# Kernel tuning notes

Measured on AMD Instinct MI355X. Metric: run time of the kernel, lower is better.

Reference implementation:

```python
import jax, jax.numpy as jnp
from jax import lax
import numpy as np

DT = jnp.float32
M = 1000          # quadrature points (torch.linspace steps=1000)
PI = float(np.pi)
EPS = 1e-12       # guards sqrt args against round-off (original asserts instead)


def _trapz(f, x):
    dx = x[1:] - x[:-1]
    return jnp.sum(0.5 * (f[..., 1:] + f[..., :-1]) * dx, axis=-1)


def _ygrid():
    return jnp.linspace(0.001, 0.999, M, dtype=DT)


def _extend(y, integ):
    # prepend linearly-extrapolated value at y=0, append 0 at y=1 (as in torch code)
    slope = (integ[..., 1] - integ[..., 0]) / (y[1] - y[0])
    v0 = integ[..., 0] - slope * y[0]
    yy = jnp.concatenate([jnp.zeros((1,), DT), y, jnp.ones((1,), DT)])
    zrs = jnp.zeros(integ.shape[:-1] + (1,), DT)
    ii = jnp.concatenate([v0[..., None], integ, zrs], axis=-1)
    return yy, ii


def eval_f(a, z):
    _a = jnp.concatenate([jnp.ones((1,), DT), a])  # [1, a0, a1]
    out = jnp.zeros_like(z)
    for i in range(3):
        for j in range(3):
            c = _a[i] * _a[j]
            if i + j == 4:
                out = out - 4.0 * c * z**4 * jnp.log(z)
            else:
                out = out + 4.0 * c * (z**4 - z**(i + j)) / (i + j - 4)
    return out


def eval_df(a, z):
    _a = jnp.concatenate([jnp.ones((1,), DT), a])
    out = jnp.zeros_like(z)
    for i in range(3):
        for j in range(3):
            out = out - 4.0 * _a[i] * _a[j] * z**(i + j)
    return (out + 4.0 * eval_f(a, z)) / z


def _bcoef(a, b):
    last = a.sum() - b.sum()
    return jnp.concatenate([jnp.ones((1,), DT), b, last[None]])  # length 4


def eval_b_(a, b, z):
    c = _bcoef(a, b)
    out = jnp.zeros_like(z)
    for i in range(4):
        for j in range(4):
            out = out + c[i] * c[j] * z**(i + j)
    return out


def eval_db(a, b, z):
    c = _bcoef(a, b)
    x = jnp.zeros_like(z)
    dx = jnp.zeros_like(z)
    for i in range(4):
        x = x + c[i] * z**i
    for i in range(1, 4):
        dx = dx + i * c[i] * z**(i - 1)
    return 2.0 * dx * x


def eval_g(a, b, z):
    return eval_b_(a, b, z) / ((1 - z) * (1 + z) * (1 + z**2))


def eval_dg(a, b, z):
    D = (1 - z) * (1 + z) * (1 + z**2)  # = 1 - z^4
    return eval_db(a, b, z) / D + 4.0 * z**3 * eval_b_(a, b, z) / D**2


def integrate_L(a, b, zs):
    y = _ygrid()
    zs_ = zs[..., None]
    z = zs_ * (1 - y) * (1 + y)
    sqrtg = jnp.sqrt(eval_g(a, b, z))
    f_over_fs = eval_f(a, z) / eval_f(a, zs_)
    arg = f_over_fs / ((1 - y)**4 * (1 + y)**4) - 1.0
    integ = sqrtg / jnp.sqrt(jnp.maximum(arg, EPS)) * y
    yy, ii = _extend(y, integ)
    return 4.0 * zs * _trapz(ii, yy) / PI


def integrate_dL(a, b, zs):
    y = _ygrid()
    zs_ = zs[..., None]
    z = zs_ * (1 - y) * (1 + y)
    fs = eval_f(a, zs_)
    g = eval_g(a, b, z)
    f_over_fs = eval_f(a, z) / fs
    df = eval_df(a, z)
    dfs = eval_df(a, zs_)
    dg = eval_dg(a, b, z)
    r4 = zs_**4 / z**4
    integ = r4 * f_over_fs * (zs_ * dfs / fs + 2 + z * dg / g) - zs_**4 / z**3 * df / fs - 2 - z * dg / g
    integ = integ * 2 * jnp.sqrt(jnp.maximum(1 - z / zs_, 0.0)) * jnp.sqrt(g) / jnp.maximum(r4 * f_over_fs - 1, EPS)**1.5
    yy, ii = _extend(y, integ)
    return _trapz(ii, yy) / PI


def integrate_V(a, b, logcoef, zs):
    coef = jnp.exp(logcoef)
    # connected piece
    y = _ygrid()
    zs_ = zs[..., None]
    z = zs_ * (1 - y) * (1 + y)
    f = eval_f(a, z)
    fg = f * eval_g(a, b, z)
    f_over_fs = f / eval_f(a, zs_)
    w = (1 - y)**2 * (1 + y)**2
    integ = jnp.sqrt(jnp.maximum(fg, EPS)) / w * (1.0 / jnp.sqrt(jnp.maximum(1 - w**2 / f_over_fs, EPS)) - 1.0) * y
    yy, ii = _extend(y, integ)
    Vc = coef * PI * 4.0 * _trapz(ii, yy) / zs
    # disconnected piece
    y2 = jnp.linspace(0.001, 1.0, M, dtype=DT)
    z2 = 1 - (1 - zs_) * y2
    fg2 = eval_f(a, z2) * eval_g(a, b, z2)
    integ2 = jnp.sqrt(jnp.maximum(fg2, EPS)) / z2**2
    yy2 = jnp.concatenate([jnp.zeros((1,), DT), y2])
    ii2 = jnp.concatenate([jnp.ones(integ2.shape[:-1] + (1,), DT), integ2], axis=-1)
    Vd = coef * PI * 2.0 * (1 - zs) * _trapz(ii2, yy2)
    return Vc - Vd


def _bisect(fun, lo, hi, iters=30):
    # keeps invariant fun(lo) >= 0 > fun(hi); matches the torch bisections
    def body(_, c):
        lo, hi = c
        mid = 0.5 * (lo + hi)
        pred = fun(mid) < 0
        return (jnp.where(pred, lo, mid), jnp.where(pred, mid, hi))
    lo, hi = lax.fori_loop(0, iters, body, (jnp.asarray(lo, DT), jnp.asarray(hi, DT)))
    return 0.5 * (lo + hi)


def get_L_max(a, b):
    zs = _bisect(lambda m: integrate_dL(a, b, m), 0.001, 0.999)
    return zs, integrate_L(a, b, zs)


def get_L_crit(a, b, logcoef, zs_max):
    zs = _bisect(lambda m: -integrate_V(a, b, logcoef, m), 0.001, zs_max)
    return zs, integrate_L(a, b, zs)


def find_zs_newton(a, b, L, init, steps=25):
    @jax.checkpoint
    def step(zs, _):
        Lz = integrate_L(a, b, zs)
        dL = integrate_dL(a, b, zs)
        zs = jnp.clip(zs - (Lz - L) / dL, 1e-4, 0.9995)
        return zs, None
    zs, _ = lax.scan(step, init, None, length=steps)
    return zs


def forward(Ls, a, b, logcoef):
    # bisection searches run under torch.no_grad in the original -> stop gradients
    a_ng = lax.stop_gradient(a)
    b_ng = lax.stop_gradient(b)
    lc_ng = lax.stop_gradient(logcoef)
    zs_max, L_max = get_L_max(a_ng, b_ng)
    zs_crit, L_crit = get_L_crit(a_ng, b_ng, lc_ng, zs_max)
    valid = Ls < L_crit
    L_eff = jnp.where(valid, Ls, 0.5 * L_crit)  # masked rows still solve a well-posed problem
    init = jnp.clip(L_eff / L_max * zs_max, 1e-4, 0.9995)  # interp1d through (0,0)-(L_max, zs_max)
    zs = find_zs_newton(a, b, L_eff, init)
    V = integrate_V(a, b, logcoef, zs)
    return jnp.where(valid, V, jnp.zeros_like(V))


def setup_inputs() -> dict:
    key = jax.random.key(0)
    k1, k2, k3 = jax.random.split(key, 3)
    B = 4096
    Ls = jax.random.uniform(k1, (B,), dtype=jnp.float32) * 0.2
    a = 0.05 * jax.random.normal(k2, (2,), dtype=jnp.float32)
    b = 0.05 * jax.random.normal(k3, (2,), dtype=jnp.float32)
    logcoef = jnp.zeros((), jnp.float32)
    return {"Ls": Ls, "a": a, "b": b, "logcoef": logcoef}


def reference(Ls, a, b, logcoef):
    return forward(Ls, a, b, logcoef)
```

## Files before the change

### kernel.cpp

```cpp
#include <hip/hip_runtime.h>
#include <math.h>

#define MQ 1000
#define PI_F 3.14159265358979323846f
#define EPSF 1e-12f
#define DYF  ((float)(0.998/999.0))
#define DY2F ((float)(0.999/999.0))
#define NG   2048
#define HG   (0.998f / (float)NG)

__device__ __forceinline__ float frcp(float x)  { return __builtin_amdgcn_rcpf(x); }
__device__ __forceinline__ float frsq(float x)  { return __builtin_amdgcn_rsqf(x); }
__device__ __forceinline__ float fsqrt(float x) { return __builtin_amdgcn_sqrtf(x); }


struct Co {
    float q1, q2, q3, q4, cf4;
    float e1, e2, e3, e4;
    float b0, b1, p3;
    float coef;
};

__device__ __forceinline__ Co make_co(const float* a, const float* b, const float* lc) {
    Co c;
    float a0 = a[0], a1 = a[1];
    float cf1 = -8.f * a0 / 3.f;
    float cf2 = -2.f * (2.f * a1 + a0 * a0);
    float cf3 = -8.f * a0 * a1;
    c.cf4 = -4.f * a1 * a1;
    c.q1 = -cf1; c.q2 = -cf2; c.q3 = -cf3; c.q4 = cf1 + cf2 + cf3 - 1.f;
    c.e1 = 2.f * a0;
    c.e2 = 2.f * a1 + a0 * a0;
    c.e3 = 2.f * a0 * a1;
    c.e4 = a1 * a1;
    c.b0 = b[0]; c.b1 = b[1];
    c.p3 = a0 + a1 - b[0] - b[1];
    c.coef = expf(lc[0]);
    return c;
}

struct Uni { float zs, fs, rfs, A4; };

__device__ __forceinline__ Uni make_uni(const Co& c, float zs) {
    Uni U; U.zs = zs;
    float z = zs;
    float lg = __logf(z);
    float t4 = c.q4 + c.cf4 * lg;
    float fz = 1.f + z * (c.q1 + z * (c.q2 + z * (c.q3 + z * t4)));
    float s  = 1.f + z * (c.e1 + z * (c.e2 + z * (c.e3 + z * c.e4)));
    U.fs = fz;
    U.rfs = frcp(fz);
    float dfs = 4.f * (fz - s) * frcp(z);
    U.A4 = zs * dfs * U.rfs - 2.f;
    return U;
}

__device__ __forceinline__ void point_LdL(const Co& c, const Uni& U,
                                          float y, float u,
                                          float& iL, float& iD) {
    float u2  = u * u;
    float ru2 = frcp(u2);
    float ru4 = ru2 * ru2;
    float z  = U.zs * u;
    float z2 = z * z, z4 = z2 * z2;
    float lg = __logf(z);
    float t4 = c.q4 + c.cf4 * lg;
    float fz = 1.f + z * (c.q1 + z * (c.q2 + z * (c.q3 + z * t4)));
    float s  = 1.f + z * (c.e1 + z * (c.e2 + z * (c.e3 + z * c.e4)));
    float P  = 1.f + z * (c.b0 + z * (c.b1 + z * c.p3));
    float dP = c.b0 + z * (2.f * c.b1 + z * (3.f * c.p3));
    float D  = 1.f - z4;
    float rsqD = frsq(D);
    float rcpD = rsqD * rsqD;
    float rcpP = frcp(P);
    float zdgg = 2.f * z * dP * rcpP + 4.f * z4 * rcpD;
    float F4 = fz * U.rfs * ru4;
    float S4 = s  * U.rfs * ru4;
    float den = fmaxf(F4 - 1.f, EPSF);
    float rs  = frsq(den);
    float sqg = P * rsqD;
    float t1  = sqg * rs;
    iL = t1 * y;
    float t = F4 * (U.A4 + zdgg) + 4.f * S4 - 2.f - zdgg;
    float rs2 = rs * rs;
    iD = t * (2.f * y) * (t1 * rs2);
}

__device__ __forceinline__ float point_Vc(const Co& c, const Uni& U,
                                          float y, float u) {
    float u2  = u * u;
    float u4  = u2 * u2;
    float ru2 = frcp(u2);
    float z  = U.zs * u;
    float z2 = z * z, z4 = z2 * z2;
    float lg = __logf(z);
    float t4 = c.q4 + c.cf4 * lg;
    float fz = 1.f + z * (c.q1 + z * (c.q2 + z * (c.q3 + z * t4)));
    float P  = 1.f + z * (c.b0 + z * (c.b1 + z * c.p3));
    float D  = 1.f - z4;
    float rsqD = frsq(D);
    float rcpD = rsqD * rsqD;
    float fg = fz * P * P * rcpD;
    float sqfg = fsqrt(fmaxf(fg, EPSF));
    float rfz = frcp(fz);
    float arg = fmaxf(1.f - u4 * U.fs * rfz, EPSF);
    float t = frsq(arg) - 1.f;
    return sqfg * ru2 * t * y;
}

__device__ __forceinline__ float point_Vd(const Co& c, const Uni& U, float y2) {
    float z  = 1.f - (1.f - U.zs) * y2;
    float z2 = z * z, z4 = z2 * z2;
    float lg = __logf(z);
    float t4 = c.q4 + c.cf4 * lg;
    float fz = 1.f + z * (c.q1 + z * (c.q2 + z * (c.q3 + z * t4)));
    float P  = 1.f + z * (c.b0 + z * (c.b1 + z * c.p3));
    float D  = 1.f - z4;
    float rsqD = frsq(D);
    float fg = fz * P * P * (rsqD * rsqD);
    float sq = fsqrt(fmaxf(fg, EPSF));
    float rz = frcp(z);
    return sq * rz * rz;
}

__device__ __forceinline__ float trapz_ext(float S, float i0, float i1, float iN) {
    float slope = (i1 - i0) * frcp(DYF);
    float v0 = i0 - slope * 0.001f;
    float yLast = 0.001f + 999.f * DYF;
    return DYF * (S - 0.5f * (i0 + iN))
         + 0.5f * (v0 + i0) * 0.001f
         + 0.5f * iN * (1.f - yLast);
}

__device__ __forceinline__ float trapz_d(float S, float q0, float qN) {
    return 0.5f * (1.f + q0) * 0.001f + DY2F * (S - 0.5f * (q0 + qN));
}

__device__ __forceinline__ void wave_LdL(const Co& c, const Uni& U, int lane,
                                         float& Lout, float& dLout) {
    float sL = 0.f, sD = 0.f, l0 = 0.f, d0 = 0.f, lN = 0.f, dN = 0.f;
#pragma unroll
    for (int k = 0; k < 16; ++k) {
        if (k < 15 || lane < 40) {
            int j = lane + 64 * k;
            float y = fmaf((float)j, DYF, 0.001f);
            float u = 1.f - y * y;
            float iL, iD;
            point_LdL(c, U, y, u, iL, iD);
            sL += iL; sD += iD;
            if (k == 0)  { l0 = iL; d0 = iD; }
            if (k == 15) { lN = iL; dN = iD; }
        }
    }
#pragma unroll
    for (int o = 32; o > 0; o >>= 1) {
        sL += __shfl_xor(sL, o, 64);
        sD += __shfl_xor(sD, o, 64);
    }
    float i0 = __shfl(l0, 0, 64), i1 = __shfl(l0, 1, 64), iN = __shfl(lN, 39, 64);
    float e0 = __shfl(d0, 0, 64), e1 = __shfl(d0, 1, 64), eN = __shfl(dN, 39, 64);
    Lout  = 4.f * U.zs * trapz_ext(sL, i0, i1, iN) / PI_F;
    dLout = trapz_ext(sD, e0, e1, eN) / PI_F;
}

__device__ __forceinline__ float wave_V(const Co& c, const Uni& U, int lane) {
    float sc = 0.f, sd = 0.f, c0 = 0.f, cN = 0.f, q0 = 0.f, qN = 0.f;
#pragma unroll
    for (int k = 0; k < 16; ++k) {
        if (k < 15 || lane < 40) {
            int j = lane + 64 * k;
            float y = fmaf((float)j, DYF, 0.001f);
            float u = 1.f - y * y;
            float vc = point_Vc(c, U, y, u);
            float y2 = fmaf((float)j, DY2F, 0.001f);
            float vd = point_Vd(c, U, y2);
            sc += vc; sd += vd;
            if (k == 0)  { c0 = vc; q0 = vd; }
            if (k == 15) { cN = vc; qN = vd; }
        }
    }
#pragma unroll
    for (int o = 32; o > 0; o >>= 1) {
        sc += __shfl_xor(sc, o, 64);
        sd += __shfl_xor(sd, o, 64);
    }
    float i0 = __shfl(c0, 0, 64), i1 = __shfl(c0, 1, 64), iN = __shfl(cN, 39, 64);
    float p0 = __shfl(q0, 0, 64), pN = __shfl(qN, 39, 64);
    float Vc = c.coef * PI_F * 4.f * trapz_ext(sc, i0, i1, iN) * frcp(U.zs);
    float Vd = c.coef * PI_F * 2.f * (1.f - U.zs) * trapz_d(sd, p0, pN);
    return Vc - Vd;
}

__global__ __launch_bounds__(256) void grid_eval_kernel(
        const float* a, const float* b, const float* lc, float* ws) {
    int wid = (blockIdx.x * blockDim.x + threadIdx.x) >> 6;
    int lane = threadIdx.x & 63;
    if (wid >= 2 * NG) return;
    Co c = make_co(a, b, lc);
    int i = (wid < NG) ? wid : wid - NG;
    float zq = fmaf((float)i + 0.5f, HG, 0.001f);
    Uni U = make_uni(c, zq);
    if (wid < NG) {
        float Lv, dLv;
        wave_LdL(c, U, lane, Lv, dLv);
        if (lane == 0) { ws[16 + i] = dLv; ws[16 + 2 * NG + i] = Lv; }
    } else {
        float v = wave_V(c, U, lane);
        if (lane == 0) ws[16 + NG + i] = v;
    }
}

__global__ __launch_bounds__(256) void scan_kernel(float* ws) {
    __shared__ int sdl, sv;
    const float* dLbuf = ws + 16;
    const float* Vbuf  = ws + 16 + NG;
    const float* Lbuf  = ws + 16 + 2 * NG;
    int t = threadIdx.x;
    if (t == 0) { sdl = NG; sv = NG; }
    __syncthreads();
#pragma unroll
    for (int r = 0; r < NG / 256; ++r) {
        int i = t + 256 * r;
        float dcur = dLbuf[i];
        float dprev = (i > 0) ? dLbuf[i - 1] : 1.f;
        if (dcur < 0.f && dprev >= 0.f) atomicMin(&sdl, i);
        float vcur = Vbuf[i];
        float vprev = (i > 0) ? Vbuf[i - 1] : -1.f;
        if (vcur > 0.f && vprev <= 0.f) atomicMin(&sv, i);
    }
    __syncthreads();
    if (t == 0) {
        int bound = sdl, iv = sv;
        float Lcrit;
        if (bound < 2) {
            Lcrit = -1.f;
        } else if (iv >= NG || iv >= bound) {
            Lcrit = Lbuf[bound - 1];
        } else if (iv == 0) {
            float z0 = 0.001f + 0.5f * HG;
            Lcrit = Lbuf[0] * 0.001f * frcp(z0);
        } else {
            float zhi = fmaf((float)iv + 0.5f, HG, 0.001f);
            float zlo = zhi - HG;
            float vhi = Vbuf[iv], vlo = Vbuf[iv - 1];
            float zc = zlo - vlo * (zhi - zlo) * frcp(fmaxf(vhi - vlo, 1e-30f));
            zc = fminf(fmaxf(zc, zlo), zhi);
            float tt = (zc - 0.001f) * frcp(HG) - 0.5f;
            int i0 = (int)tt;
            i0 = max(0, min(i0, bound - 2));
            float frac = fminf(fmaxf(tt - (float)i0, 0.f), 1.f);
            Lcrit = Lbuf[i0] + frac * (Lbuf[i0 + 1] - Lbuf[i0]);
        }
        ws[0] = Lcrit;
        ws[1] = (float)bound;
    }
}

__global__ __launch_bounds__(256) void elem_v_kernel(
        const float* Ls, const float* a, const float* b, const float* lc,
        const float* ws, float* out, int B) {
    int wid = (blockIdx.x * blockDim.x + threadIdx.x) >> 6;
    int lane = threadIdx.x & 63;
    if (wid >= B) return;

    float L_crit = ws[0];
    int bound = (int)ws[1];
    float Lq = Ls[wid];
    if (!(Lq < L_crit)) {
        if (lane == 0) out[wid] = 0.f;
        return;
    }

    const float* Lbuf = ws + 16 + 2 * NG;
    int lo = -1, hi = bound - 1;
    while (hi > lo) {
        int mid = (lo + hi + 1) >> 1;
        if (Lbuf[mid] < Lq) lo = mid; else hi = mid - 1;
    }
    float zs;
    if (lo < 0) {
        float z0 = 0.001f + 0.5f * HG;
        zs = z0 * Lq * frcp(fmaxf(Lbuf[0], 1e-20f));
    } else {
        int seg = min(lo, bound - 2);
        float zl = fmaf((float)seg + 0.5f, HG, 0.001f);
        float Ll = Lbuf[seg], Lh = Lbuf[seg + 1];
        zs = zl + (Lq - Ll) * HG * frcp(fmaxf(Lh - Ll, 1e-20f));
    }
    zs = fminf(fmaxf(zs, 1e-4f), 0.9995f);

    Co c = make_co(a, b, lc);
    Uni U = make_uni(c, zs);
    float Lz, dL;
    wave_LdL(c, U, lane, Lz, dL);
    float delta = (Lz - Lq) * frcp(dL);
    if (fabsf(delta) <= 2.f * HG)
        zs = fminf(fmaxf(zs - delta, 1e-4f), 0.9995f);

    U = make_uni(c, zs);
    float V = wave_V(c, U, lane);
    if (lane == 0) out[wid] = V;
}

extern "C" void kernel_launch(void* const* d_in, const int* in_sizes, int n_in,
                              void* d_out, int out_size, void* d_ws, size_t ws_size,
                              hipStream_t stream) {
    const float* Ls = (const float*)d_in[0];
    const float* a  = (const float*)d_in[1];
    const float* b  = (const float*)d_in[2];
    const float* lc = (const float*)d_in[3];
    float* out = (float*)d_out;
    float* ws  = (float*)d_ws;
    int B = in_sizes[0];

    int blocksA = (2 * NG * 64) / 256;
    grid_eval_kernel<<<blocksA, 256, 0, stream>>>(a, b, lc, ws);
    scan_kernel<<<1, 256, 0, stream>>>(ws);

    int blocksC = (B + 3) / 4;
    elem_v_kernel<<<blocksC, 256, 0, stream>>>(Ls, a, b, lc, ws, out, B);
}
```

Baseline: 97.26 us.

## Replace per-element Newton step with Hermite interpolation and use two-wave blocks per point

The per-element kernel no longer runs the extra full L/dL quadrature plus Newton correction. It instead refines the initial zs by Hermite cubic interpolation of the precomputed L grid using the stored dL derivatives, two Newton iterations on the cubic. This removes roughly a third of that kernel's quadrature work. Separately, each grid point and each batch element now uses a 128-thread block with two waves and a shared-memory reduction, in place of one 64-lane wave with 16 points per lane. Accuracy now depends on how well the Hermite interpolant fits, and the extra LDS sync adds some overhead.

```diff
diff --git a/kernel.cpp b/kernel.cpp
--- a/kernel.cpp
+++ b/kernel.cpp
@@ -136,77 +136,89 @@
     return 0.5f * (1.f + q0) * 0.001f + DY2F * (S - 0.5f * (q0 + qN));
 }
 
-__device__ __forceinline__ void wave_LdL(const Co& c, const Uni& U, int lane,
-                                         float& Lout, float& dLout) {
-    float sL = 0.f, sD = 0.f, l0 = 0.f, d0 = 0.f, lN = 0.f, dN = 0.f;
-#pragma unroll
-    for (int k = 0; k < 16; ++k) {
-        if (k < 15 || lane < 40) {
-            int j = lane + 64 * k;
-            float y = fmaf((float)j, DYF, 0.001f);
-            float u = 1.f - y * y;
-            float iL, iD;
-            point_LdL(c, U, y, u, iL, iD);
-            sL += iL; sD += iD;
-            if (k == 0)  { l0 = iL; d0 = iD; }
-            if (k == 15) { lN = iL; dN = iD; }
-        }
-    }
-#pragma unroll
-    for (int o = 32; o > 0; o >>= 1) {
-        sL += __shfl_xor(sL, o, 64);
-        sD += __shfl_xor(sD, o, 64);
-    }
-    float i0 = __shfl(l0, 0, 64), i1 = __shfl(l0, 1, 64), iN = __shfl(lN, 39, 64);
-    float e0 = __shfl(d0, 0, 64), e1 = __shfl(d0, 1, 64), eN = __shfl(dN, 39, 64);
-    Lout  = 4.f * U.zs * trapz_ext(sL, i0, i1, iN) / PI_F;
-    dLout = trapz_ext(sD, e0, e1, eN) / PI_F;
-}
-
-__device__ __forceinline__ float wave_V(const Co& c, const Uni& U, int lane) {
-    float sc = 0.f, sd = 0.f, c0 = 0.f, cN = 0.f, q0 = 0.f, qN = 0.f;
-#pragma unroll
-    for (int k = 0; k < 16; ++k) {
-        if (k < 15 || lane < 40) {
-            int j = lane + 64 * k;
-            float y = fmaf((float)j, DYF, 0.001f);
-            float u = 1.f - y * y;
-            float vc = point_Vc(c, U, y, u);
-            float y2 = fmaf((float)j, DY2F, 0.001f);
-            float vd = point_Vd(c, U, y2);
-            sc += vc; sd += vd;
-            if (k == 0)  { c0 = vc; q0 = vd; }
-            if (k == 15) { cN = vc; qN = vd; }
-        }
-    }
-#pragma unroll
-    for (int o = 32; o > 0; o >>= 1) {
-        sc += __shfl_xor(sc, o, 64);
-        sd += __shfl_xor(sd, o, 64);
-    }
-    float i0 = __shfl(c0, 0, 64), i1 = __shfl(c0, 1, 64), iN = __shfl(cN, 39, 64);
-    float p0 = __shfl(q0, 0, 64), pN = __shfl(qN, 39, 64);
-    float Vc = c.coef * PI_F * 4.f * trapz_ext(sc, i0, i1, iN) * frcp(U.zs);
-    float Vd = c.coef * PI_F * 2.f * (1.f - U.zs) * trapz_d(sd, p0, pN);
-    return Vc - Vd;
-}
-
-__global__ __launch_bounds__(256) void grid_eval_kernel(
+__global__ __launch_bounds__(128) void grid_eval_kernel(
         const float* a, const float* b, const float* lc, float* ws) {
-    int wid = (blockIdx.x * blockDim.x + threadIdx.x) >> 6;
-    int lane = threadIdx.x & 63;
-    if (wid >= 2 * NG) return;
+    __shared__ float red[4];
+    __shared__ float spx[8];
+    int bid = blockIdx.x;
+    int t = threadIdx.x, lane = t & 63, w = t >> 6;
     Co c = make_co(a, b, lc);
-    int i = (wid < NG) ? wid : wid - NG;
+    int i = (bid < NG) ? bid : bid - NG;
     float zq = fmaf((float)i + 0.5f, HG, 0.001f);
     Uni U = make_uni(c, zq);
-    if (wid < NG) {
-        float Lv, dLv;
-        wave_LdL(c, U, lane, Lv, dLv);
-        if (lane == 0) { ws[16 + i] = dLv; ws[16 + 2 * NG + i] = Lv; }
+
+    if (bid < NG) {
+        float sL = 0.f, sD = 0.f, l0 = 0.f, d0 = 0.f, l1 = 0.f, d1 = 0.f,
+              lN = 0.f, dN = 0.f;
+#pragma unroll
+        for (int k = 0; k < 8; ++k) {
+            if (k < 7 || t < 104) {
+                int j = t + 128 * k;
+                float y = fmaf((float)j, DYF, 0.001f);
+                float u = 1.f - y * y;
+                float iL, iD;
+                point_LdL(c, U, y, u, iL, iD);
+                sL += iL; sD += iD;
+                if (k == 0) {
+                    if (t == 0) { l0 = iL; d0 = iD; }
+                    if (t == 1) { l1 = iL; d1 = iD; }
+                }
+                if (k == 7 && t == 103) { lN = iL; dN = iD; }
+            }
+        }
+#pragma unroll
+        for (int o = 32; o > 0; o >>= 1) {
+            sL += __shfl_xor(sL, o, 64);
+            sD += __shfl_xor(sD, o, 64);
+        }
+        if (lane == 0) { red[w] = sL; red[2 + w] = sD; }
+        if (t == 0)   { spx[0] = l0; spx[3] = d0; }
+        if (t == 1)   { spx[1] = l1; spx[4] = d1; }
+        if (t == 103) { spx[2] = lN; spx[5] = dN; }
+        __syncthreads();
+        if (t == 0) {
+            float SL = red[0] + red[1], SD = red[2] + red[3];
+            float Lv  = 4.f * zq * trapz_ext(SL, spx[0], spx[1], spx[2]) / PI_F;
+            float dLv = trapz_ext(SD, spx[3], spx[4], spx[5]) / PI_F;
+            ws[16 + i] = dLv;
+            ws[16 + 2 * NG + i] = Lv;
+        }
     } else {
-        float v = wave_V(c, U, lane);
-        if (lane == 0) ws[16 + NG + i] = v;
+        float sc = 0.f, sd = 0.f, c0 = 0.f, c1v = 0.f, cN = 0.f,
+              q0 = 0.f, qN = 0.f;
+#pragma unroll
+        for (int k = 0; k < 8; ++k) {
+            if (k < 7 || t < 104) {
+                int j = t + 128 * k;
+                float y = fmaf((float)j, DYF, 0.001f);
+                float u = 1.f - y * y;
+                float vc = point_Vc(c, U, y, u);
+                float y2 = fmaf((float)j, DY2F, 0.001f);
+                float vd = point_Vd(c, U, y2);
+                sc += vc; sd += vd;
+                if (k == 0) {
+                    if (t == 0) { c0 = vc; q0 = vd; }
+                    if (t == 1) { c1v = vc; }
+                }
+                if (k == 7 && t == 103) { cN = vc; qN = vd; }
+            }
+        }
+#pragma unroll
+        for (int o = 32; o > 0; o >>= 1) {
+            sc += __shfl_xor(sc, o, 64);
+            sd += __shfl_xor(sd, o, 64);
+        }
+        if (lane == 0) { red[w] = sc; red[2 + w] = sd; }
+        if (t == 0)   { spx[0] = c0; spx[3] = q0; }
+        if (t == 1)   { spx[1] = c1v; }
+        if (t == 103) { spx[2] = cN; spx[4] = qN; }
+        __syncthreads();
+        if (t == 0) {
+            float Sc = red[0] + red[1], Sd = red[2] + red[3];
+            float Vc = c.coef * PI_F * 4.f * trapz_ext(Sc, spx[0], spx[1], spx[2]) * frcp(zq);
+            float Vd = c.coef * PI_F * 2.f * (1.f - zq) * trapz_d(Sd, spx[3], spx[4]);
+            ws[16 + NG + i] = Vc - Vd;
+        }
     }
 }
 
@@ -256,22 +268,25 @@
     }
 }
 
-__global__ __launch_bounds__(256) void elem_v_kernel(
+__global__ __launch_bounds__(128) void elem_v_kernel(
         const float* Ls, const float* a, const float* b, const float* lc,
         const float* ws, float* out, int B) {
-    int wid = (blockIdx.x * blockDim.x + threadIdx.x) >> 6;
-    int lane = threadIdx.x & 63;
+    __shared__ float red[4];
+    __shared__ float spx[8];
+    int wid = blockIdx.x;
+    int t = threadIdx.x, lane = t & 63, w = t >> 6;
     if (wid >= B) return;
 
     float L_crit = ws[0];
     int bound = (int)ws[1];
     float Lq = Ls[wid];
-    if (!(Lq < L_crit)) {
-        if (lane == 0) out[wid] = 0.f;
+    if (!(Lq < L_crit) || bound < 2) {
+        if (t == 0) out[wid] = 0.f;
         return;
     }
 
-    const float* Lbuf = ws + 16 + 2 * NG;
+    const float* dLbuf = ws + 16;
+    const float* Lbuf  = ws + 16 + 2 * NG;
     int lo = -1, hi = bound - 1;
     while (hi > lo) {
         int mid = (lo + hi + 1) >> 1;
@@ -284,22 +299,59 @@
     } else {
         int seg = min(lo, bound - 2);
         float zl = fmaf((float)seg + 0.5f, HG, 0.001f);
-        float Ll = Lbuf[seg], Lh = Lbuf[seg + 1];
-        zs = zl + (Lq - Ll) * HG * frcp(fmaxf(Lh - Ll, 1e-20f));
+        float Ll = Lbuf[seg],  Lh = Lbuf[seg + 1];
+        float dl = dLbuf[seg] * HG, dh = dLbuf[seg + 1] * HG;
+        float s = fminf(fmaxf((Lq - Ll) * frcp(fmaxf(Lh - Ll, 1e-20f)), 0.f), 1.f);
+#pragma unroll
+        for (int it = 0; it < 2; ++it) {
+            float s2 = s * s, s3 = s2 * s;
+            float H  = (2.f*s3 - 3.f*s2 + 1.f) * Ll + (s3 - 2.f*s2 + s) * dl
+                     + (-2.f*s3 + 3.f*s2) * Lh + (s3 - s2) * dh;
+            float Hp = (6.f*s2 - 6.f*s) * (Ll - Lh)
+                     + (3.f*s2 - 4.f*s + 1.f) * dl + (3.f*s2 - 2.f*s) * dh;
+            float step = (H - Lq) * frcp(Hp);
+            if (fabsf(Hp) > 1e-20f) s = fminf(fmaxf(s - step, 0.f), 1.f);
+        }
+        zs = fmaf(s, HG, zl);
     }
     zs = fminf(fmaxf(zs, 1e-4f), 0.9995f);
 
     Co c = make_co(a, b, lc);
     Uni U = make_uni(c, zs);
-    float Lz, dL;
-    wave_LdL(c, U, lane, Lz, dL);
-    float delta = (Lz - Lq) * frcp(dL);
-    if (fabsf(delta) <= 2.f * HG)
-        zs = fminf(fmaxf(zs - delta, 1e-4f), 0.9995f);
-
-    U = make_uni(c, zs);
-    float V = wave_V(c, U, lane);
-    if (lane == 0) out[wid] = V;
+    float sc = 0.f, sd = 0.f, c0 = 0.f, c1v = 0.f, cN = 0.f, q0 = 0.f, qN = 0.f;
+#pragma unroll
+    for (int k = 0; k < 8; ++k) {
+        if (k < 7 || t < 104) {
+            int j = t + 128 * k;
+            float y = fmaf((float)j, DYF, 0.001f);
+            float u = 1.f - y * y;
+            float vc = point_Vc(c, U, y, u);
+            float y2 = fmaf((float)j, DY2F, 0.001f);
+            float vd = point_Vd(c, U, y2);
+            sc += vc; sd += vd;
+            if (k == 0) {
+                if (t == 0) { c0 = vc; q0 = vd; }
+                if (t == 1) { c1v = vc; }
+            }
+            if (k == 7 && t == 103) { cN = vc; qN = vd; }
+        }
+    }
+#pragma unroll
+    for (int o = 32; o > 0; o >>= 1) {
+        sc += __shfl_xor(sc, o, 64);
+        sd += __shfl_xor(sd, o, 64);
+    }
+    if (lane == 0) { red[w] = sc; red[2 + w] = sd; }
+    if (t == 0)   { spx[0] = c0; spx[3] = q0; }
+    if (t == 1)   { spx[1] = c1v; }
+    if (t == 103) { spx[2] = cN; spx[4] = qN; }
+    __syncthreads();
+    if (t == 0) {
+        float Sc = red[0] + red[1], Sd = red[2] + red[3];
+        float Vc = c.coef * PI_F * 4.f * trapz_ext(Sc, spx[0], spx[1], spx[2]) * frcp(zs);
+        float Vd = c.coef * PI_F * 2.f * (1.f - zs) * trapz_d(Sd, spx[3], spx[4]);
+        out[wid] = Vc - Vd;
+    }
 }
 
 extern "C" void kernel_launch(void* const* d_in, const int* in_sizes, int n_in,
@@ -313,10 +365,7 @@
     float* ws  = (float*)d_ws;
     int B = in_sizes[0];
 
-    int blocksA = (2 * NG * 64) / 256;
-    grid_eval_kernel<<<blocksA, 256, 0, stream>>>(a, b, lc, ws);
+    grid_eval_kernel<<<2 * NG, 128, 0, stream>>>(a, b, lc, ws);
     scan_kernel<<<1, 256, 0, stream>>>(ws);
-
-    int blocksC = (B + 3) / 4;
-    elem_v_kernel<<<blocksC, 256, 0, stream>>>(Ls, a, b, lc, ws, out, B);
-}
+    elem_v_kernel<<<B, 128, 0, stream>>>(Ls, a, b, lc, ws, out, B);
+}
```

Measured after the change: 94.64 us. 1.03x faster.
